# Kernel tuning notes

Measured on AMD Instinct MI355X. Metric: run time of the kernel, lower is better.

Reference implementation:

```python
import jax, jax.numpy as jnp
import numpy as np


def setup_inputs() -> dict:
    key = jax.random.key(0)
    kK, kV, kQ = jax.random.split(key, 3)
    B, D, S = 4, 64, 4096
    K = jax.random.normal(kK, (B, D, S), dtype=jnp.float32)
    V = jax.random.normal(kV, (B, D, S), dtype=jnp.float32)
    Q = jax.random.normal(kQ, (B, D, S), dtype=jnp.float32)
    return {"K": K, "V": V, "Q": Q}


def reference(K, V, Q):
    # K,V: [B, D, Sk], Q: [B, D, Sq]
    d = Q.shape[1]
    # A[b,k,q] = sum_d K[b,d,k] * Q[b,d,q] / sqrt(d)
    A = jnp.einsum("bdk,bdq->bkq", K, Q) / jnp.sqrt(jnp.asarray(d, Q.dtype))
    A = jax.nn.softmax(A, axis=1)  # normalize over keys (dim 1), matching F.softmax(A, 1)
    # R[b,d,q] = sum_k V[b,d,k] * A[b,k,q]
    R = jnp.einsum("bdk,bkq->bdq", V, A)
    return jnp.concatenate((R, Q), axis=1)  # [B, 2D, Sq]
```

## Files before the change

kernel.cpp:

```cpp
#include <hip/hip_runtime.h>
#include <hip/hip_bf16.h>

#define S_LEN 4096
#define D_DIM 64
#define QB 128
#define KB 32
#define NT (S_LEN / KB)
#define TILE_E 4096

typedef __attribute__((ext_vector_type(8)))  short bf16x8;
typedef __attribute__((ext_vector_type(16))) float f32x16;
typedef unsigned int u32;

#define Z16 {0.f,0.f,0.f,0.f,0.f,0.f,0.f,0.f,0.f,0.f,0.f,0.f,0.f,0.f,0.f,0.f}

union bpack8 { __hip_bfloat16 h[8]; bf16x8 v; };
union ppack  { u32 w[4]; bf16x8 v; };
union bload4 { uint2 u; __hip_bfloat16 h[4]; };

static __device__ __forceinline__ float fexp2(float x) {
    return __builtin_amdgcn_exp2f(x);
}
static __device__ __forceinline__ u32 cvtpk(float lo, float hi) {
    u32 r;
    asm("v_cvt_pk_bf16_f32 %0, %1, %2" : "=v"(r) : "v"(lo), "v"(hi));
    return r;
}
static __device__ __forceinline__ void plswap(u32 &a, u32 &b) {
    asm("v_permlane32_swap_b32 %0, %1" : "+v"(a), "+v"(b));
}

#define GLD16(gp, lp) __builtin_amdgcn_global_load_lds( \
    (const __attribute__((address_space(1))) u32*)(const void*)(gp), \
    (__attribute__((address_space(3))) u32*)(void*)(lp), 16, 0, 0)

#define QSCALE 0.18033688011112042f

__global__ __launch_bounds__(256)
void prep_all(const float* __restrict__ K, const float* __restrict__ V,
              const float* __restrict__ Q,
              __hip_bfloat16* __restrict__ KVbf, __hip_bfloat16* __restrict__ Qbf,
              float* __restrict__ out)
{
    const int b = blockIdx.y, x = blockIdx.x, z = blockIdx.z;
    const int t = threadIdx.x;

    if (z == 0) {
        const int key = t & 31, dg = t >> 5;
        const float* src = K + ((size_t)b * D_DIM + dg * 8) * S_LEN + x * KB + key;
        bpack8 u;
        #pragma unroll
        for (int e = 0; e < 8; ++e)
            u.h[e] = __float2bfloat16(src[(size_t)e * S_LEN]);
        *(bf16x8*)&KVbf[((size_t)b * NT + x) * TILE_E + t * 8] = u.v;
    } else if (z == 1) {
        const int kg = t >> 6, d = t & 63;
        const float* p = V + ((size_t)b * D_DIM + d) * S_LEN + x * KB + kg * 8;
        float4 a = *(const float4*)p, c = *(const float4*)(p + 4);
        bpack8 u;
        u.h[0] = __float2bfloat16(a.x); u.h[1] = __float2bfloat16(a.y);
        u.h[2] = __float2bfloat16(a.z); u.h[3] = __float2bfloat16(a.w);
        u.h[4] = __float2bfloat16(c.x); u.h[5] = __float2bfloat16(c.y);
        u.h[6] = __float2bfloat16(c.z); u.h[7] = __float2bfloat16(c.w);
        *(bf16x8*)&KVbf[((size_t)b * NT + x) * TILE_E + 2048 + t * 8] = u.v;
    } else {
        const int q = x * 32 + (t & 31), dg = t >> 5;
        const float* src = Q + ((size_t)b * D_DIM + dg * 8) * S_LEN + q;
        float r[8];
        #pragma unroll
        for (int e = 0; e < 8; ++e) r[e] = src[(size_t)e * S_LEN];
        float* o = out + ((size_t)b * 2 * D_DIM + D_DIM + dg * 8) * S_LEN + q;
        #pragma unroll
        for (int e = 0; e < 8; ++e) o[(size_t)e * S_LEN] = r[e];
        bpack8 u;
        #pragma unroll
        for (int e = 0; e < 8; ++e) u.h[e] = __float2bfloat16(r[e] * QSCALE);
        *(bf16x8*)&Qbf[((size_t)b * S_LEN + q) * D_DIM + dg * 8] = u.v;
    }
}

__global__ __launch_bounds__(256, 5)
void attn_fwd(const __hip_bfloat16* __restrict__ KVbf,
              const __hip_bfloat16* __restrict__ Qbf,
              float* __restrict__ out,
              __hip_bfloat16* __restrict__ accPb, float* __restrict__ lP,
              int base, int rem, int nb, int direct)
{
    const int b  = blockIdx.y;
    const int z  = blockIdx.z;
    const int q0 = blockIdx.x * QB;

    const int t    = threadIdx.x;
    const int lane = t & 63;
    const int w    = t >> 6;
    const int l5   = lane & 31;
    const int h    = lane >> 5;

    __shared__ __align__(16) char Ls[2][8192];

    const int tile0  = z * base + (z < rem ? z : rem);
    const int ntiles = base + (z < rem ? 1 : 0);
    const __hip_bfloat16* kvb = KVbf + ((size_t)b * NT + tile0) * TILE_E;

    const __hip_bfloat16* qrow = Qbf + ((size_t)b * S_LEN + q0 + w * 32 + l5) * D_DIM;
    bf16x8 qf[4];
    #pragma unroll
    for (int j = 0; j < 4; ++j)
        qf[j] = *(const bf16x8*)&qrow[(2 * j + h) * 8];

    GLD16(kvb + w * 512 + lane * 8,        Ls[0] + w * 1024);
    GLD16(kvb + 2048 + w * 512 + lane * 8, Ls[0] + 4096 + w * 1024);
    __syncthreads();

    float lsum = 0.f;
    f32x16 acc[2] = {Z16, Z16};
    int cur = 0;

    for (int it = 0; it < ntiles; ++it) {
        if (it + 1 < ntiles) {
            const __hip_bfloat16* nx = kvb + (size_t)(it + 1) * TILE_E;
            GLD16(nx + w * 512 + lane * 8,        Ls[cur ^ 1] + w * 1024);
            GLD16(nx + 2048 + w * 512 + lane * 8, Ls[cur ^ 1] + 4096 + w * 1024);
        }
        const char* Lk = Ls[cur];
        const char* Lv = Ls[cur] + 4096;

        f32x16 s = Z16;
        __builtin_amdgcn_s_setprio(1);
        #pragma unroll
        for (int j = 0; j < 4; ++j) {
            bf16x8 kf = *(const bf16x8*)(Lk + ((2 * j + h) * 32 + l5) * 16);
            s = __builtin_amdgcn_mfma_f32_32x32x16_bf16(kf, qf[j], s, 0, 0, 0);
        }
        __builtin_amdgcn_s_setprio(0);

        float e[16];
        #pragma unroll
        for (int r = 0; r < 16; ++r) e[r] = fexp2(s[r]);
        float ps = 0.f;
        #pragma unroll
        for (int r = 0; r < 16; ++r) ps += e[r];
        lsum += ps;

        u32 A = cvtpk(e[0],  e[1]),  Bw = cvtpk(e[2],  e[3]);
        u32 C = cvtpk(e[4],  e[5]),  Dw = cvtpk(e[6],  e[7]);
        u32 E = cvtpk(e[8],  e[9]),  F  = cvtpk(e[10], e[11]);
        u32 G = cvtpk(e[12], e[13]), H  = cvtpk(e[14], e[15]);
        plswap(A, C); plswap(Bw, Dw); plswap(E, G); plswap(F, H);
        ppack pf[2];
        pf[0].w[0] = A; pf[0].w[1] = Bw; pf[0].w[2] = C; pf[0].w[3] = Dw;
        pf[1].w[0] = E; pf[1].w[1] = F;  pf[1].w[2] = G; pf[1].w[3] = H;

        __builtin_amdgcn_s_setprio(1);
        #pragma unroll
        for (int j = 0; j < 2; ++j)
            #pragma unroll
            for (int dt = 0; dt < 2; ++dt) {
                bf16x8 vf = *(const bf16x8*)(Lv + ((2 * j + h) * 64 + dt * 32 + l5) * 16);
                acc[dt] = __builtin_amdgcn_mfma_f32_32x32x16_bf16(vf, pf[j].v, acc[dt], 0, 0, 0);
            }
        __builtin_amdgcn_s_setprio(0);

        __syncthreads();
        cur ^= 1;
    }

    lsum += __shfl_xor(lsum, 32);

    const int qcol = q0 + w * 32 + l5;
    if (!direct) {
        __hip_bfloat16* ap = accPb + (size_t)(z * nb + b) * D_DIM * S_LEN;
        #pragma unroll
        for (int dt = 0; dt < 2; ++dt)
            #pragma unroll
            for (int r = 0; r < 16; ++r) {
                int d = dt * 32 + (r & 3) + 8 * (r >> 2) + 4 * h;
                ap[(size_t)d * S_LEN + qcol] = __float2bfloat16(acc[dt][r]);
            }
        if (h == 0)
            lP[(size_t)(z * nb + b) * S_LEN + qcol] = lsum;
    } else {
        float inv = 1.f / lsum;
        float* op = out + (size_t)b * 2 * D_DIM * S_LEN;
        #pragma unroll
        for (int dt = 0; dt < 2; ++dt)
            #pragma unroll
            for (int r = 0; r < 16; ++r) {
                int d = dt * 32 + (r & 3) + 8 * (r >> 2) + 4 * h;
                op[(size_t)d * S_LEN + qcol] = acc[dt][r] * inv;
            }
    }
}

__global__ __launch_bounds__(256)
void attn_combine(const __hip_bfloat16* __restrict__ accPb,
                  const float* __restrict__ lP,
                  float* __restrict__ out, int nsplit, int nb)
{
    int gid = blockIdx.x * 256 + threadIdx.x;
    int q4   = gid & (S_LEN / 4 - 1);
    int rest = gid >> 10;
    int d    = rest & (D_DIM - 1);
    int b    = rest >> 6;
    if (b >= nb) return;
    size_t qoff = (size_t)q4 * 4;

    float num[4] = {0.f,0.f,0.f,0.f}, den[4] = {0.f,0.f,0.f,0.f};
    for (int z = 0; z < nsplit; ++z) {
        bload4 a;
        a.u = *(const uint2*)&accPb[((size_t)(z * nb + b) * D_DIM + d) * S_LEN + qoff];
        float4 lz = *(const float4*)&lP[(size_t)(z * nb + b) * S_LEN + qoff];
        num[0] += __bfloat162float(a.h[0]); num[1] += __bfloat162float(a.h[1]);
        num[2] += __bfloat162float(a.h[2]); num[3] += __bfloat162float(a.h[3]);
        den[0] += lz.x; den[1] += lz.y; den[2] += lz.z; den[3] += lz.w;
    }
    float4 r;
    r.x = num[0] / den[0]; r.y = num[1] / den[1];
    r.z = num[2] / den[2]; r.w = num[3] / den[3];
    *(float4*)&out[((size_t)b * 2 * D_DIM + d) * S_LEN + qoff] = r;
}

extern "C" void kernel_launch(void* const* d_in, const int* in_sizes, int n_in,
                              void* d_out, int out_size, void* d_ws, size_t ws_size,
                              hipStream_t stream) {
    const float* K = (const float*)d_in[0];
    const float* V = (const float*)d_in[1];
    const float* Q = (const float*)d_in[2];
    float* out = (float*)d_out;

    const int B = in_sizes[0] / (D_DIM * S_LEN);
    const size_t kvE = (size_t)B * NT * TILE_E;
    const size_t qE  = (size_t)B * S_LEN * D_DIM;

    auto need = [&](int ns) -> size_t {
        return (kvE + qE) * 2
             + (size_t)ns * B * D_DIM * S_LEN * 2
             + (size_t)ns * B * S_LEN * 4;
    };
    const int cand[6] = {10, 8, 5, 4, 2, 1};
    int nsplit = 1;
    for (int i = 0; i < 6; ++i)
        if (need(cand[i]) <= ws_size) { nsplit = cand[i]; break; }
    const int direct = (nsplit == 1);

    __hip_bfloat16* KVbf = (__hip_bfloat16*)d_ws;
    __hip_bfloat16* Qbf  = KVbf + kvE;
    __hip_bfloat16* accPb = Qbf + qE;
    float* lP = (float*)(accPb + (size_t)nsplit * B * D_DIM * S_LEN);

    const int base = NT / nsplit, rem = NT % nsplit;

    prep_all<<<dim3(NT, B, 3), dim3(256), 0, stream>>>(K, V, Q, KVbf, Qbf, out);

    attn_fwd<<<dim3(S_LEN / QB, B, nsplit), dim3(256), 0, stream>>>(
        KVbf, Qbf, out, accPb, lP, base, rem, B, direct);

    if (!direct) {
        int total = B * D_DIM * (S_LEN / 4);
        attn_combine<<<dim3(total / 256), dim3(256), 0, stream>>>(
            accPb, lP, out, nsplit, B);
    }
}
```

Before: 39.52 us.

## Process two KV tiles per pipeline stage to halve barriers

```diff
diff --git a/kernel.cpp b/kernel.cpp
--- a/kernel.cpp
+++ b/kernel.cpp
@@ -79,12 +79,12 @@
     }
 }
 
-__global__ __launch_bounds__(256, 5)
+__global__ __launch_bounds__(256, 4)
 void attn_fwd(const __hip_bfloat16* __restrict__ KVbf,
               const __hip_bfloat16* __restrict__ Qbf,
               float* __restrict__ out,
               __hip_bfloat16* __restrict__ accPb, float* __restrict__ lP,
-              int base, int rem, int nb, int direct)
+              int ntiles, int nb, int direct)
 {
     const int b  = blockIdx.y;
     const int z  = blockIdx.z;
@@ -96,11 +96,9 @@
     const int l5   = lane & 31;
     const int h    = lane >> 5;
 
-    __shared__ __align__(16) char Ls[2][8192];
-
-    const int tile0  = z * base + (z < rem ? z : rem);
-    const int ntiles = base + (z < rem ? 1 : 0);
-    const __hip_bfloat16* kvb = KVbf + ((size_t)b * NT + tile0) * TILE_E;
+    __shared__ __align__(16) char Ls[2][16384];
+
+    const __hip_bfloat16* kvb = KVbf + ((size_t)b * NT + z * ntiles) * TILE_E;
 
     const __hip_bfloat16* qrow = Qbf + ((size_t)b * S_LEN + q0 + w * 32 + l5) * D_DIM;
     bf16x8 qf[4];
@@ -108,58 +106,73 @@
     for (int j = 0; j < 4; ++j)
         qf[j] = *(const bf16x8*)&qrow[(2 * j + h) * 8];
 
-    GLD16(kvb + w * 512 + lane * 8,        Ls[0] + w * 1024);
-    GLD16(kvb + 2048 + w * 512 + lane * 8, Ls[0] + 4096 + w * 1024);
+    #pragma unroll
+    for (int sub = 0; sub < 2; ++sub) {
+        GLD16(kvb + sub * TILE_E + t * 8,        Ls[0] + sub * 8192 + w * 1024);
+        GLD16(kvb + sub * TILE_E + 2048 + t * 8, Ls[0] + sub * 8192 + 4096 + w * 1024);
+    }
     __syncthreads();
 
     float lsum = 0.f;
     f32x16 acc[2] = {Z16, Z16};
     int cur = 0;
 
-    for (int it = 0; it < ntiles; ++it) {
-        if (it + 1 < ntiles) {
-            const __hip_bfloat16* nx = kvb + (size_t)(it + 1) * TILE_E;
-            GLD16(nx + w * 512 + lane * 8,        Ls[cur ^ 1] + w * 1024);
-            GLD16(nx + 2048 + w * 512 + lane * 8, Ls[cur ^ 1] + 4096 + w * 1024);
+    const int npairs = ntiles >> 1;
+    for (int p = 0; p < npairs; ++p) {
+        if (p + 1 < npairs) {
+            const __hip_bfloat16* nx = kvb + (size_t)(2 * p + 2) * TILE_E;
+            #pragma unroll
+            for (int sub = 0; sub < 2; ++sub) {
+                GLD16(nx + sub * TILE_E + t * 8,
+                      Ls[cur ^ 1] + sub * 8192 + w * 1024);
+                GLD16(nx + sub * TILE_E + 2048 + t * 8,
+                      Ls[cur ^ 1] + sub * 8192 + 4096 + w * 1024);
+            }
         }
-        const char* Lk = Ls[cur];
-        const char* Lv = Ls[cur] + 4096;
-
-        f32x16 s = Z16;
-        __builtin_amdgcn_s_setprio(1);
-        #pragma unroll
-        for (int j = 0; j < 4; ++j) {
-            bf16x8 kf = *(const bf16x8*)(Lk + ((2 * j + h) * 32 + l5) * 16);
-            s = __builtin_amdgcn_mfma_f32_32x32x16_bf16(kf, qf[j], s, 0, 0, 0);
+
+        #pragma unroll
+        for (int sub = 0; sub < 2; ++sub) {
+            const char* Lk = Ls[cur] + sub * 8192;
+            const char* Lv = Lk + 4096;
+
+            f32x16 s = Z16;
+            __builtin_amdgcn_s_setprio(1);
+            #pragma unroll
+            for (int j = 0; j < 4; ++j) {
+                bf16x8 kf = *(const bf16x8*)(Lk + ((2 * j + h) * 32 + l5) * 16);
+                s = __builtin_amdgcn_mfma_f32_32x32x16_bf16(kf, qf[j], s, 0, 0, 0);
+            }
+            __builtin_amdgcn_s_setprio(0);
+
+            #pragma unroll
+            for (int r = 0; r < 16; ++r) s[r] = fexp2(s[r]);
+            {
+                float a0 = (s[0] + s[1])   + (s[2] + s[3]);
+                float a1 = (s[4] + s[5])   + (s[6] + s[7]);
+                float a2 = (s[8] + s[9])   + (s[10] + s[11]);
+                float a3 = (s[12] + s[13]) + (s[14] + s[15]);
+                lsum += (a0 + a1) + (a2 + a3);
+            }
+
+            u32 A = cvtpk(s[0],  s[1]),  Bw = cvtpk(s[2],  s[3]);
+            u32 C = cvtpk(s[4],  s[5]),  Dw = cvtpk(s[6],  s[7]);
+            u32 E = cvtpk(s[8],  s[9]),  F  = cvtpk(s[10], s[11]);
+            u32 G = cvtpk(s[12], s[13]), H  = cvtpk(s[14], s[15]);
+            plswap(A, C); plswap(Bw, Dw); plswap(E, G); plswap(F, H);
+            ppack pf[2];
+            pf[0].w[0] = A; pf[0].w[1] = Bw; pf[0].w[2] = C; pf[0].w[3] = Dw;
+            pf[1].w[0] = E; pf[1].w[1] = F;  pf[1].w[2] = G; pf[1].w[3] = H;
+
+            __builtin_amdgcn_s_setprio(1);
+            #pragma unroll
+            for (int j = 0; j < 2; ++j)
+                #pragma unroll
+                for (int dt = 0; dt < 2; ++dt) {
+                    bf16x8 vf = *(const bf16x8*)(Lv + ((2 * j + h) * 64 + dt * 32 + l5) * 16);
+                    acc[dt] = __builtin_amdgcn_mfma_f32_32x32x16_bf16(vf, pf[j].v, acc[dt], 0, 0, 0);
+                }
+            __builtin_amdgcn_s_setprio(0);
         }
-        __builtin_amdgcn_s_setprio(0);
-
-        float e[16];
-        #pragma unroll
-        for (int r = 0; r < 16; ++r) e[r] = fexp2(s[r]);
-        float ps = 0.f;
-        #pragma unroll
-        for (int r = 0; r < 16; ++r) ps += e[r];
-        lsum += ps;
-
-        u32 A = cvtpk(e[0],  e[1]),  Bw = cvtpk(e[2],  e[3]);
-        u32 C = cvtpk(e[4],  e[5]),  Dw = cvtpk(e[6],  e[7]);
-        u32 E = cvtpk(e[8],  e[9]),  F  = cvtpk(e[10], e[11]);
-        u32 G = cvtpk(e[12], e[13]), H  = cvtpk(e[14], e[15]);
-        plswap(A, C); plswap(Bw, Dw); plswap(E, G); plswap(F, H);
-        ppack pf[2];
-        pf[0].w[0] = A; pf[0].w[1] = Bw; pf[0].w[2] = C; pf[0].w[3] = Dw;
-        pf[1].w[0] = E; pf[1].w[1] = F;  pf[1].w[2] = G; pf[1].w[3] = H;
-
-        __builtin_amdgcn_s_setprio(1);
-        #pragma unroll
-        for (int j = 0; j < 2; ++j)
-            #pragma unroll
-            for (int dt = 0; dt < 2; ++dt) {
-                bf16x8 vf = *(const bf16x8*)(Lv + ((2 * j + h) * 64 + dt * 32 + l5) * 16);
-                acc[dt] = __builtin_amdgcn_mfma_f32_32x32x16_bf16(vf, pf[j].v, acc[dt], 0, 0, 0);
-            }
-        __builtin_amdgcn_s_setprio(0);
 
         __syncthreads();
         cur ^= 1;
@@ -237,9 +250,9 @@
              + (size_t)ns * B * D_DIM * S_LEN * 2
              + (size_t)ns * B * S_LEN * 4;
     };
-    const int cand[6] = {10, 8, 5, 4, 2, 1};
+    const int cand[4] = {8, 4, 2, 1};
     int nsplit = 1;
-    for (int i = 0; i < 6; ++i)
+    for (int i = 0; i < 4; ++i)
         if (need(cand[i]) <= ws_size) { nsplit = cand[i]; break; }
     const int direct = (nsplit == 1);
 
@@ -248,12 +261,10 @@
     __hip_bfloat16* accPb = Qbf + qE;
     float* lP = (float*)(accPb + (size_t)nsplit * B * D_DIM * S_LEN);
 
-    const int base = NT / nsplit, rem = NT % nsplit;
-
     prep_all<<<dim3(NT, B, 3), dim3(256), 0, stream>>>(K, V, Q, KVbf, Qbf, out);
 
     attn_fwd<<<dim3(S_LEN / QB, B, nsplit), dim3(256), 0, stream>>>(
-        KVbf, Qbf, out, accPb, lP, base, rem, B, direct);
+        KVbf, Qbf, out, accPb, lP, NT / nsplit, B, direct);
 
     if (!direct) {
         int total = B * D_DIM * (S_LEN / 4);
```

After: 38.09 us. 3.6% less time.
